# Optimization experiments

Hardware: AMD Instinct MI355X
Metric: run time of the kernel (lower is better)

Reference implementation:

```python
import jax, jax.numpy as jnp
import numpy as np

B, P, R_BAR, WIDTH, ADD_WIDTH, KERNEL_WIDTH = 4096, 1024, 64, 1024, 64, 16
NEG_SLOPE = 0.1

def leaky(x):
    return jnp.where(x > 0, x, NEG_SLOPE * x)

def setup_inputs() -> dict:
    key = jax.random.key(0)
    ks = jax.random.split(key, 16)
    s = lambda fan_in: 1.0 / np.sqrt(fan_in)
    return {
        "x": jax.random.normal(ks[0], (B, P), jnp.float32),
        # PCA layer 1: Linear(p -> r_bar), stored [in, out]
        "W_pca": jax.random.normal(ks[1], (P, R_BAR), jnp.float32) * s(P),
        "b_pca": jnp.zeros((R_BAR,), jnp.float32),
        # relu_stack: Linear(r_bar -> width), Linear(width -> width)
        "W1": jax.random.normal(ks[2], (R_BAR, WIDTH), jnp.float32) * s(R_BAR),
        "b1": jnp.zeros((WIDTH,), jnp.float32),
        "W2": jax.random.normal(ks[3], (WIDTH, WIDTH), jnp.float32) * s(WIDTH),
        "b2": jnp.zeros((WIDTH,), jnp.float32),
        # AdditiveLayer 1: r_bar tiny Linears (kernel_width -> add_width), batched [r, in, out]
        "add1_W": jax.random.normal(ks[4], (R_BAR, KERNEL_WIDTH, ADD_WIDTH), jnp.float32) * s(KERNEL_WIDTH),
        "add1_b": jnp.zeros((R_BAR, ADD_WIDTH), jnp.float32),
        "add1_bias": jnp.zeros((1,), jnp.float32),
        # AdditiveLayer 2: r_bar Linears (add_width -> add_width)
        "add2_W": jax.random.normal(ks[5], (R_BAR, ADD_WIDTH, ADD_WIDTH), jnp.float32) * s(ADD_WIDTH),
        "add2_b": jnp.zeros((R_BAR, ADD_WIDTH), jnp.float32),
        "add2_bias": jnp.zeros((1,), jnp.float32),
        # PCA layer 2: Linear(r_bar*add_width -> r_bar)
        "W_pca2": jax.random.normal(ks[6], (R_BAR * ADD_WIDTH, R_BAR), jnp.float32) * s(R_BAR * ADD_WIDTH),
        "b_pca2": jnp.zeros((R_BAR,), jnp.float32),
        # last layer: Linear(r_bar -> 1)
        "W_last": jax.random.normal(ks[7], (R_BAR, 1), jnp.float32) * s(R_BAR),
        "b_last": jnp.zeros((1,), jnp.float32),
    }

def reference(x, W_pca, b_pca, W1, b1, W2, b2,
              add1_W, add1_b, add1_bias,
              add2_W, add2_b, add2_bias,
              W_pca2, b_pca2, W_last, b_last):
    # PcaLayer 1 (cov/trace bookkeeping does not affect the output)
    t = x @ W_pca + b_pca                                   # [B, r_bar]
    # relu_stack (nn_depth = 2)
    h = leaky(t @ W1 + b1)                                   # [B, width]
    h = leaky(h @ W2 + b2)                                   # [B, width]
    # AdditiveLayer 1: modulo-gather kernel_width cols per slot, batched tiny GEMMs
    idx1 = jnp.arange(R_BAR * KERNEL_WIDTH) % h.shape[1]
    g1 = h[:, idx1].reshape(-1, R_BAR, KERNEL_WIDTH)         # [B, r, kw]
    a = jnp.einsum('brk,rko->bro', g1, add1_W) + add1_b      # [B, r, add_w]
    a = leaky(a.reshape(a.shape[0], -1) + add1_bias)         # [B, r*add_w]
    # AdditiveLayer 2: slices are contiguous (mod is identity) -> plain reshape
    g2 = a.reshape(-1, R_BAR, ADD_WIDTH)
    a2 = jnp.einsum('bri,rio->bro', g2, add2_W) + add2_b
    a2 = leaky(a2.reshape(a2.shape[0], -1) + add2_bias)      # [B, r*add_w]
    # PcaLayer 2 + last layer
    t2 = a2 @ W_pca2 + b_pca2                                # [B, r_bar]
    out = (t2 @ W_last + b_last).reshape(-1, 1)              # [B, 1]
    return out
```

## Files before the change

### kernel.cpp

```cpp
#include <hip/hip_runtime.h>

#define NEG_SLOPE 0.1f

__device__ __forceinline__ float leaky(float v) { return v > 0.0f ? v : NEG_SLOPE * v; }

typedef _Float16 h4_t __attribute__((ext_vector_type(4)));
typedef _Float16 h8_t __attribute__((ext_vector_type(8)));
typedef float f32x4 __attribute__((ext_vector_type(4)));

__device__ __forceinline__ unsigned lds_off(const void* p) {
    return (unsigned)(unsigned long long)p;
}

__device__ __forceinline__ void lgkm0() {
    asm volatile("s_waitcnt lgkmcnt(0)" ::: "memory");
    __builtin_amdgcn_sched_barrier(0);
}

__device__ __forceinline__ h4_t tr16(unsigned addr) {
    h4_t d;
    asm volatile("ds_read_b64_tr_b16 %0, %1" : "=v"(d) : "v"(addr) : "memory");
    return d;
}

__global__ __launch_bounds__(256) void prep_and_splitk(const float* __restrict__ W2,
                                                       const float* __restrict__ W1,
                                                       const float* __restrict__ a1W,
                                                       const float* __restrict__ a2W,
                                                       const float* __restrict__ Wp2,
                                                       const float* __restrict__ x,
                                                       const float* __restrict__ Wpca,
                                                       _Float16* __restrict__ W2T,
                                                       _Float16* __restrict__ W1T,
                                                       _Float16* __restrict__ wpack,
                                                       float* __restrict__ P)
{
    __shared__ float tile[32][33];
    __shared__ alignas(16) float As[32][33];
    __shared__ alignas(16) float Bs[32][64];
    const int b   = blockIdx.x;
    const int tid = threadIdx.x;

    if (b < 1024) {
        const int n0 = (b & 31) * 32, k0 = (b >> 5) * 32;
        const int r = tid >> 3, c4 = (tid & 7) * 4;
        float4 v = *reinterpret_cast<const float4*>(&W2[(size_t)(k0 + r) * 1024 + n0 + c4]);
        tile[r][c4 + 0] = v.x; tile[r][c4 + 1] = v.y;
        tile[r][c4 + 2] = v.z; tile[r][c4 + 3] = v.w;
        __syncthreads();
        h4_t o;
        o[0] = (_Float16)tile[c4 + 0][r]; o[1] = (_Float16)tile[c4 + 1][r];
        o[2] = (_Float16)tile[c4 + 2][r]; o[3] = (_Float16)tile[c4 + 3][r];
        *reinterpret_cast<h4_t*>(&W2T[(size_t)(n0 + r) * 1024 + k0 + c4]) = o;
    } else if (b < 1088) {
        const int b2 = b - 1024;
        const int n0 = (b2 & 31) * 32, k0 = (b2 >> 5) * 32;
        const int r = tid >> 3, c4 = (tid & 7) * 4;
        float4 v = *reinterpret_cast<const float4*>(&W1[(size_t)(k0 + r) * 1024 + n0 + c4]);
        tile[r][c4 + 0] = v.x; tile[r][c4 + 1] = v.y;
        tile[r][c4 + 2] = v.z; tile[r][c4 + 3] = v.w;
        __syncthreads();
        h4_t o;
        o[0] = (_Float16)tile[c4 + 0][r]; o[1] = (_Float16)tile[c4 + 1][r];
        o[2] = (_Float16)tile[c4 + 2][r]; o[3] = (_Float16)tile[c4 + 3][r];
        *reinterpret_cast<h4_t*>(&W1T[(size_t)(n0 + r) * 64 + k0 + c4]) = o;
    } else if (b < 3392) {
        const int idx = (b - 1088) * 256 + tid;
        if (idx < 589824) {
            const int r = idx / 9216, qq = idx % 9216;
            float v;
            if (qq < 1024) {
                int nt = qq >> 8, rem = qq & 255, l = rem >> 2, j = rem & 3;
                int n = nt * 16 + (l & 15), k = (l >> 4) * 4 + j;
                v = a1W[(size_t)r * 1024 + k * 64 + n];
            } else if (qq < 5120) {
                int p = qq - 1024, kt = p >> 11, u = p & 2047, nt = u >> 9, s = u & 511,
                    l = s >> 3, j = s & 7;
                int n = nt * 16 + (l & 15), k = kt * 32 + (l >> 4) * 8 + j;
                v = a2W[(size_t)r * 4096 + k * 64 + n];
            } else {
                int p = qq - 5120, kt = p >> 11, u = p & 2047, nt = u >> 9, s = u & 511,
                    l = s >> 3, j = s & 7;
                int n = nt * 16 + (l & 15), k = kt * 32 + (l >> 4) * 8 + j;
                v = Wp2[((size_t)r * 64 + k) * 64 + n];
            }
            wpack[idx] = (_Float16)v;
        }
    } else {
        const int b2    = b - 3392;
        const int row0  = (b2 & 127) * 32;
        const int kbase = (b2 >> 7) * 128;
        const int r0    = (tid >> 4) * 2;
        const int c0    = (tid & 15) * 4;
        const int am    = tid >> 3;
        const int ak    = (tid & 7) * 4;
        float acc[2][4] = {};

#pragma unroll
        for (int kc = 0; kc < 128; kc += 32) {
            const int k0 = kbase + kc;
            float4 va = *reinterpret_cast<const float4*>(&x[(size_t)(row0 + am) * 1024 + k0 + ak]);
            As[ak + 0][am] = va.x; As[ak + 1][am] = va.y;
            As[ak + 2][am] = va.z; As[ak + 3][am] = va.w;
#pragma unroll
            for (int p = 0; p < 2; ++p) {
                int idx = tid + p * 256;
                int kk  = idx >> 4;
                int nq  = (idx & 15) * 4;
                *reinterpret_cast<float4*>(&Bs[kk][nq]) =
                    *reinterpret_cast<const float4*>(&Wpca[(size_t)(k0 + kk) * 64 + nq]);
            }
            __syncthreads();
#pragma unroll
            for (int k = 0; k < 32; ++k) {
                float a0 = As[k][r0], a1 = As[k][r0 + 1];
                float4 bv = *reinterpret_cast<const float4*>(&Bs[k][c0]);
                acc[0][0] = fmaf(a0, bv.x, acc[0][0]); acc[0][1] = fmaf(a0, bv.y, acc[0][1]);
                acc[0][2] = fmaf(a0, bv.z, acc[0][2]); acc[0][3] = fmaf(a0, bv.w, acc[0][3]);
                acc[1][0] = fmaf(a1, bv.x, acc[1][0]); acc[1][1] = fmaf(a1, bv.y, acc[1][1]);
                acc[1][2] = fmaf(a1, bv.z, acc[1][2]); acc[1][3] = fmaf(a1, bv.w, acc[1][3]);
            }
            __syncthreads();
        }
#pragma unroll
        for (int i = 0; i < 2; ++i) {
            float4 o; o.x = acc[i][0]; o.y = acc[i][1]; o.z = acc[i][2]; o.w = acc[i][3];
            *reinterpret_cast<float4*>(
                &P[((size_t)(b2 >> 7) * 4096 + row0 + r0 + i) * 64 + c0]) = o;
        }
    }
}

__global__ __launch_bounds__(256) void combine_t16(const float* __restrict__ P,
                                                   const float* __restrict__ bias,
                                                   _Float16* __restrict__ t16)
{
    const int idx = blockIdx.x * 256 + threadIdx.x;
    float s = bias[idx & 63];
#pragma unroll
    for (int c = 0; c < 8; ++c)
        s += P[(size_t)c * 262144 + idx];
    t16[idx] = (_Float16)s;
}

__global__ __launch_bounds__(256) void gemm_k64_mfma(const _Float16* __restrict__ A,
                                                     const _Float16* __restrict__ BT,
                                                     const float* __restrict__ bias,
                                                     _Float16* __restrict__ C)
{
    __shared__ alignas(16) _Float16 As[128 * 64];
    __shared__ alignas(16) _Float16 Bs[128 * 64];
    const int tid = threadIdx.x;
    const int l   = tid & 63;
    const int w   = tid >> 6;
    const int wm  = w >> 1;
    const int wn  = w & 1;
    const int bm0 = blockIdx.y * 128;
    const int bn0 = blockIdx.x * 128;
    const int fr  = l & 15;
    const int fg  = l >> 4;
    const int srow  = l >> 3;
    const int sslot = l & 7;

#pragma unroll
    for (int i = 0; i < 4; ++i) {
        const int r0   = w * 32 + i * 8;
        const int rowA = r0 + srow;
        const int slot = sslot ^ (rowA & 7);
        __builtin_amdgcn_global_load_lds(
            (const __attribute__((address_space(1))) void*)&A[(size_t)(bm0 + rowA) * 64 + slot * 8],
            (__attribute__((address_space(3))) void*)&As[r0 * 64], 16, 0, 0);
        __builtin_amdgcn_global_load_lds(
            (const __attribute__((address_space(1))) void*)&BT[(size_t)(bn0 + rowA) * 64 + slot * 8],
            (__attribute__((address_space(3))) void*)&Bs[r0 * 64], 16, 0, 0);
    }
    __syncthreads();

    f32x4 acc[4][4] = {};
#pragma unroll
    for (int ks = 0; ks < 2; ++ks) {
        h8_t af[4], bf[4];
#pragma unroll
        for (int mt = 0; mt < 4; ++mt) {
            int row = wm * 64 + mt * 16 + fr;
            int sg  = ks * 4 + fg;
            af[mt] = *reinterpret_cast<const h8_t*>(&As[row * 64 + ((sg ^ (row & 7)) << 3)]);
        }
#pragma unroll
        for (int nt = 0; nt < 4; ++nt) {
            int row = wn * 64 + nt * 16 + fr;
            int sg  = ks * 4 + fg;
            bf[nt] = *reinterpret_cast<const h8_t*>(&Bs[row * 64 + ((sg ^ (row & 7)) << 3)]);
        }
#pragma unroll
        for (int mt = 0; mt < 4; ++mt)
#pragma unroll
            for (int nt = 0; nt < 4; ++nt)
                acc[mt][nt] = __builtin_amdgcn_mfma_f32_16x16x32_f16(af[mt], bf[nt],
                                                                     acc[mt][nt], 0, 0, 0);
    }

#pragma unroll
    for (int nt = 0; nt < 4; ++nt) {
        const int col = bn0 + wn * 64 + nt * 16 + fr;
        const float bv = bias[col];
#pragma unroll
        for (int mt = 0; mt < 4; ++mt)
#pragma unroll
            for (int rg = 0; rg < 4; ++rg) {
                const int row = bm0 + wm * 64 + mt * 16 + fg * 4 + rg;
                float v = acc[mt][nt][rg] + bv;
                C[(size_t)row * 1024 + col] = (_Float16)fmaxf(v, NEG_SLOPE * v);
            }
    }
}

__global__ __launch_bounds__(256) void gemm_mfma_f16_v2(const _Float16* __restrict__ A,
                                                        const _Float16* __restrict__ BT,
                                                        const float* __restrict__ bias,
                                                        _Float16* __restrict__ h2t)
{
    __shared__ alignas(16) _Float16 As[64 * 64];
    __shared__ alignas(16) _Float16 Bs[128 * 64];
    const int tid = threadIdx.x;
    const int l   = tid & 63;
    const int w   = tid >> 6;
    const int wm  = w >> 1;
    const int wn  = w & 1;
    const int bm0 = blockIdx.y * 64;
    const int bn0 = blockIdx.x * 128;
    const int fr  = l & 15;
    const int fg  = l >> 4;
    const int srow  = l >> 3;
    const int sslot = l & 7;

    f32x4 acc[2][4] = {};

    for (int k0 = 0; k0 < 1024; k0 += 64) {
#pragma unroll
        for (int i = 0; i < 2; ++i) {
            const int r0   = w * 16 + i * 8;
            const int rowA = r0 + srow;
            const int slot = sslot ^ (rowA & 7);
            __builtin_amdgcn_global_load_lds(
                (const __attribute__((address_space(1))) void*)&A[(size_t)(bm0 + rowA) * 1024 + k0 + slot * 8],
                (__attribute__((address_space(3))) void*)&As[r0 * 64], 16, 0, 0);
        }
#pragma unroll
        for (int i = 0; i < 4; ++i) {
            const int r0   = w * 32 + i * 8;
            const int rowB = r0 + srow;
            const int slot = sslot ^ (rowB & 7);
            __builtin_amdgcn_global_load_lds(
                (const __attribute__((address_space(1))) void*)&BT[(size_t)(bn0 + rowB) * 1024 + k0 + slot * 8],
                (__attribute__((address_space(3))) void*)&Bs[r0 * 64], 16, 0, 0);
        }
        __syncthreads();

#pragma unroll
        for (int ks = 0; ks < 2; ++ks) {
            h8_t af[2], bf[4];
#pragma unroll
            for (int mt = 0; mt < 2; ++mt) {
                int row = wm * 32 + mt * 16 + fr;
                int sg  = ks * 4 + fg;
                af[mt] = *reinterpret_cast<const h8_t*>(&As[row * 64 + ((sg ^ (row & 7)) << 3)]);
            }
#pragma unroll
            for (int nt = 0; nt < 4; ++nt) {
                int row = wn * 64 + nt * 16 + fr;
                int sg  = ks * 4 + fg;
                bf[nt] = *reinterpret_cast<const h8_t*>(&Bs[row * 64 + ((sg ^ (row & 7)) << 3)]);
            }
#pragma unroll
            for (int mt = 0; mt < 2; ++mt)
#pragma unroll
                for (int nt = 0; nt < 4; ++nt)
                    acc[mt][nt] = __builtin_amdgcn_mfma_f32_16x16x32_f16(af[mt], bf[nt],
                                                                         acc[mt][nt], 0, 0, 0);
        }
        __syncthreads();
    }

    const int rblk0 = (bm0 >> 4) + wm * 2;
    const int cblk0 = (bn0 >> 4) + wn * 4;
#pragma unroll
    for (int nt = 0; nt < 4; ++nt) {
        const int col = bn0 + wn * 64 + nt * 16 + fr;
        const float bv = bias[col];
#pragma unroll
        for (int mt = 0; mt < 2; ++mt) {
            h4_t pk;
#pragma unroll
            for (int r = 0; r < 4; ++r) {
                float v = acc[mt][nt][r] + bv;
                pk[r] = (_Float16)fmaxf(v, NEG_SLOPE * v);
            }
            *reinterpret_cast<h4_t*>(
                &h2t[(((size_t)(cblk0 + nt) * 256 + rblk0 + mt) * 16 + fr) * 16 + fg * 4]) = pk;
        }
    }
}

#define RCH 4

__global__ __launch_bounds__(256) void fused_tail5(const _Float16* __restrict__ h2t,
                                                   const _Float16* __restrict__ wpack,
                                                   const float* __restrict__ a1b,
                                                   const float* __restrict__ a1bias,
                                                   const float* __restrict__ a2b,
                                                   const float* __restrict__ a2bias,
                                                   float* __restrict__ partials)
{
    __shared__ alignas(16) _Float16 stage[2][11264];
    __shared__ alignas(16) _Float16 act[4][2048];

    const int tid = threadIdx.x;
    const int l = tid & 63, w = tid >> 6;
    const int c = l & 15, q = l >> 4;
    const int row0  = blockIdx.x * 128;
    const int rbase = blockIdx.y * RCH;
    const float b1s = a1bias[0], b2s = a2bias[0];

    const unsigned trl   = l * 8;
    const unsigned abase = lds_off(&act[w][0]);

    float b1v[RCH][4], b2v[RCH][4];
#pragma unroll
    for (int rl = 0; rl < RCH; ++rl)
#pragma unroll
        for (int nt = 0; nt < 4; ++nt) {
            b1v[rl][nt] = a1b[(rbase + rl) * 64 + nt * 16 + c] + b1s;
            b2v[rl][nt] = a2b[(rbase + rl) * 64 + nt * 16 + c] + b2s;
        }

    auto STAGE = [&](int rl, int b) {
        const int r = rbase + rl;
        const _Float16* hsrc = h2t + ((size_t)r * 256 + blockIdx.x * 8) * 256;
        const _Float16* wsrc = wpack + (size_t)r * 9216;
#pragma unroll
        for (int i = 0; i < 6; ++i) {
            const int ch = i * 4 + w;
            if (ch < 22) {
                const _Float16* src = (ch < 4) ? (hsrc + ch * 512) : (wsrc + (ch - 4) * 512);
                __builtin_amdgcn_global_load_lds(
                    (const __attribute__((address_space(1))) void*)(src + l * 8),
                    (__attribute__((address_space(3))) void*)&stage[b][ch * 512], 16, 0, 0);
            }
        }
    };

    STAGE(0, 0);
    __syncthreads();

    f32x4 accT[2][4] = {};
    int cur = 0;

#pragma unroll
    for (int rl = 0; rl < RCH; ++rl) {
        if (rl + 1 < RCH) STAGE(rl + 1, cur ^ 1);

        const _Float16* sp = &stage[cur][0];
        const unsigned sbytes = lds_off(sp);

        h4_t ha0 = tr16(sbytes + (unsigned)(w) * 512 + trl);
        h4_t ha1 = tr16(sbytes + (unsigned)(w + 4) * 512 + trl);
        lgkm0();
        f32x4 pa[2][4];
#pragma unroll
        for (int nt = 0; nt < 4; ++nt) {
            h4_t bf = *reinterpret_cast<const h4_t*>(&sp[2048 + nt * 256 + l * 4]);
            pa[0][nt] = __builtin_amdgcn_mfma_f32_16x16x16f16(ha0, bf, (f32x4){0.f,0.f,0.f,0.f}, 0, 0, 0);
            pa[1][nt] = __builtin_amdgcn_mfma_f32_16x16x16f16(ha1, bf, (f32x4){0.f,0.f,0.f,0.f}, 0, 0, 0);
        }
#pragma unroll
        for (int j = 0; j < 2; ++j)
#pragma unroll
            for (int nt = 0; nt < 4; ++nt) {
                h4_t pk;
#pragma unroll
                for (int rg = 0; rg < 4; ++rg) {
                    float v = pa[j][nt][rg] + b1v[rl][nt];
                    pk[rg] = (_Float16)fmaxf(v, NEG_SLOPE * v);
                }
                const int kk = nt * 16 + c;
                const int hh = (kk >> 2) & 1;
                const int kp = (kk & 3) | ((kk >> 3) << 2);
                *reinterpret_cast<h4_t*>(&act[w][j * 1024 + hh * 512 + kp * 16 + q * 4]) = pk;
            }
        lgkm0();

        h8_t afB[2][2];
#pragma unroll
        for (int j = 0; j < 2; ++j)
#pragma unroll
            for (int kt = 0; kt < 2; ++kt) {
                h4_t lo = tr16(abase + (unsigned)(j * 2048 + kt * 512) + trl);
                h4_t hi = tr16(abase + (unsigned)(j * 2048 + 1024 + kt * 512) + trl);
                afB[j][kt] = __builtin_shufflevector(lo, hi, 0, 1, 2, 3, 4, 5, 6, 7);
            }
        lgkm0();
        f32x4 pb[2][4] = {};
#pragma unroll
        for (int kt = 0; kt < 2; ++kt)
#pragma unroll
            for (int nt = 0; nt < 4; ++nt) {
                h8_t bf = *reinterpret_cast<const h8_t*>(&sp[3072 + kt * 2048 + nt * 512 + l * 8]);
                pb[0][nt] = __builtin_amdgcn_mfma_f32_16x16x32_f16(afB[0][kt], bf, pb[0][nt], 0, 0, 0);
                pb[1][nt] = __builtin_amdgcn_mfma_f32_16x16x32_f16(afB[1][kt], bf, pb[1][nt], 0, 0, 0);
            }
#pragma unroll
        for (int j = 0; j < 2; ++j)
#pragma unroll
            for (int nt = 0; nt < 4; ++nt) {
                h4_t pk;
#pragma unroll
                for (int rg = 0; rg < 4; ++rg) {
                    float v = pb[j][nt][rg] + b2v[rl][nt];
                    pk[rg] = (_Float16)fmaxf(v, NEG_SLOPE * v);
                }
                const int kk = nt * 16 + c;
                const int hh = (kk >> 2) & 1;
                const int kp = (kk & 3) | ((kk >> 3) << 2);
                *reinterpret_cast<h4_t*>(&act[w][j * 1024 + hh * 512 + kp * 16 + q * 4]) = pk;
            }
        lgkm0();

        h8_t afC[2][2];
#pragma unroll
        for (int j = 0; j < 2; ++j)
#pragma unroll
            for (int kt = 0; kt < 2; ++kt) {
                h4_t lo = tr16(abase + (unsigned)(j * 2048 + kt * 512) + trl);
                h4_t hi = tr16(abase + (unsigned)(j * 2048 + 1024 + kt * 512) + trl);
                afC[j][kt] = __builtin_shufflevector(lo, hi, 0, 1, 2, 3, 4, 5, 6, 7);
            }
        lgkm0();
#pragma unroll
        for (int kt = 0; kt < 2; ++kt)
#pragma unroll
            for (int nt = 0; nt < 4; ++nt) {
                h8_t bf = *reinterpret_cast<const h8_t*>(&sp[7168 + kt * 2048 + nt * 512 + l * 8]);
                accT[0][nt] = __builtin_amdgcn_mfma_f32_16x16x32_f16(afC[0][kt], bf, accT[0][nt], 0, 0, 0);
                accT[1][nt] = __builtin_amdgcn_mfma_f32_16x16x32_f16(afC[1][kt], bf, accT[1][nt], 0, 0, 0);
            }

        __syncthreads();
        cur ^= 1;
    }

#pragma unroll
    for (int j = 0; j < 2; ++j)
#pragma unroll
        for (int nt = 0; nt < 4; ++nt)
#pragma unroll
            for (int rg = 0; rg < 4; ++rg)
                partials[((size_t)blockIdx.y * 4096 + row0 + (w + 4 * j) * 16 + q * 4 + rg) * 64
                         + nt * 16 + c] = accT[j][nt][rg];
}

__global__ __launch_bounds__(256) void reduce_out(const float* __restrict__ partials,
                                                  const float* __restrict__ bp2,
                                                  const float* __restrict__ Wl,
                                                  const float* __restrict__ bl,
                                                  float* __restrict__ out)
{
    const int tid = threadIdx.x;
    const int row = blockIdx.x * 4 + (tid >> 6);
    const int col = tid & 63;
    float s = bp2[col];
#pragma unroll
    for (int c = 0; c < 16; ++c)
        s += partials[(size_t)c * 262144 + (size_t)row * 64 + col];
    s *= Wl[col];
    s += __shfl_xor(s, 1);
    s += __shfl_xor(s, 2);
    s += __shfl_xor(s, 4);
    s += __shfl_xor(s, 8);
    s += __shfl_xor(s, 16);
    s += __shfl_xor(s, 32);
    if (col == 0) out[row] = s + bl[0];
}

extern "C" void kernel_launch(void* const* d_in, const int* in_sizes, int n_in,
                              void* d_out, int out_size, void* d_ws, size_t ws_size,
                              hipStream_t stream)
{
    const float* x      = (const float*)d_in[0];
    const float* Wpca   = (const float*)d_in[1];
    const float* bpca   = (const float*)d_in[2];
    const float* W1     = (const float*)d_in[3];
    const float* b1     = (const float*)d_in[4];
    const float* W2     = (const float*)d_in[5];
    const float* b2     = (const float*)d_in[6];
    const float* a1W    = (const float*)d_in[7];
    const float* a1b    = (const float*)d_in[8];
    const float* a1bias = (const float*)d_in[9];
    const float* a2W    = (const float*)d_in[10];
    const float* a2b    = (const float*)d_in[11];
    const float* a2bias = (const float*)d_in[12];
    const float* Wp2    = (const float*)d_in[13];
    const float* bp2    = (const float*)d_in[14];
    const float* Wl     = (const float*)d_in[15];
    const float* bl     = (const float*)d_in[16];
    float* out = (float*)d_out;

    char* wsb = (char*)d_ws;
    _Float16* t16      = (_Float16*)(wsb);
    _Float16* h1h      = (_Float16*)(wsb + (1ull  << 20));
    _Float16* h2t      = (_Float16*)(wsb + (9ull  << 20));
    _Float16* W2T      = (_Float16*)(wsb + (17ull << 20));
    _Float16* wpack    = (_Float16*)(wsb + (19ull << 20));
    _Float16* W1T      = (_Float16*)(wsb + (21ull << 20));
    float*    partials = (float*)   (wsb + (22ull << 20));
    float*    tpart    = (float*)   (wsb + (9ull  << 20));

    prep_and_splitk<<<dim3(4416), 256, 0, stream>>>(W2, W1, a1W, a2W, Wp2, x, Wpca,
                                                    W2T, W1T, wpack, tpart);
    combine_t16<<<dim3(1024), 256, 0, stream>>>(tpart, bpca, t16);
    gemm_k64_mfma<<<dim3(8, 32), 256, 0, stream>>>(t16, W1T, b1, h1h);
    gemm_mfma_f16_v2<<<dim3(8, 64), 256, 0, stream>>>(h1h, W2T, b2, h2t);
    fused_tail5<<<dim3(32, 16), 256, 0, stream>>>(h2t, wpack, a1b, a1bias,
                                                  a2b, a2bias, partials);
    reduce_out<<<dim3(1024), 256, 0, stream>>>(partials, bp2, Wl, bl, out);
}
```

Measured before the change: 67.14 us.

## Fuse final reduction and last layer into tail kernel via atomics

The tail kernel now projects its split-r partial PCA2 outputs through W_last inside the kernel. It reduces them across lanes with shuffles and atomically adds a scalar per row into the output. The output is pre-initialised with the constant bias term (b_last + bp2·Wl) inside the earlier combine kernel. This removes the 16 MB partials write/read and the reduce_out launch, at the cost of 16-way float atomic contention per row and nondeterministic summation order.

Result: faster. 63.95 us (-4.8%).

```diff
diff --git a/kernel.cpp b/kernel.cpp
--- a/kernel.cpp
+++ b/kernel.cpp
@@ -133,7 +133,11 @@
 
 __global__ __launch_bounds__(256) void combine_t16(const float* __restrict__ P,
                                                    const float* __restrict__ bias,
-                                                   _Float16* __restrict__ t16)
+                                                   const float* __restrict__ bp2,
+                                                   const float* __restrict__ Wl,
+                                                   const float* __restrict__ bl,
+                                                   _Float16* __restrict__ t16,
+                                                   float* __restrict__ out)
 {
     const int idx = blockIdx.x * 256 + threadIdx.x;
     float s = bias[idx & 63];
@@ -141,6 +145,14 @@
     for (int c = 0; c < 8; ++c)
         s += P[(size_t)c * 262144 + idx];
     t16[idx] = (_Float16)s;
+
+    if (idx < 4096) {
+        float cst = bl[0];
+#pragma unroll
+        for (int f = 0; f < 64; ++f)
+            cst += bp2[f] * Wl[f];
+        out[idx] = cst;
+    }
 }
 
 __global__ __launch_bounds__(256) void gemm_k64_mfma(const _Float16* __restrict__ A,
@@ -304,13 +316,14 @@
 
 #define RCH 4
 
-__global__ __launch_bounds__(256) void fused_tail5(const _Float16* __restrict__ h2t,
-                                                   const _Float16* __restrict__ wpack,
-                                                   const float* __restrict__ a1b,
-                                                   const float* __restrict__ a1bias,
-                                                   const float* __restrict__ a2b,
-                                                   const float* __restrict__ a2bias,
-                                                   float* __restrict__ partials)
+__global__ __launch_bounds__(256) void fused_tail5b(const _Float16* __restrict__ h2t,
+                                                    const _Float16* __restrict__ wpack,
+                                                    const float* __restrict__ a1b,
+                                                    const float* __restrict__ a1bias,
+                                                    const float* __restrict__ a2b,
+                                                    const float* __restrict__ a2bias,
+                                                    const float* __restrict__ Wl,
+                                                    float* __restrict__ out)
 {
     __shared__ alignas(16) _Float16 stage[2][11264];
     __shared__ alignas(16) _Float16 act[4][2048];
@@ -333,6 +346,9 @@
             b1v[rl][nt] = a1b[(rbase + rl) * 64 + nt * 16 + c] + b1s;
             b2v[rl][nt] = a2b[(rbase + rl) * 64 + nt * 16 + c] + b2s;
         }
+    float wlv[4];
+#pragma unroll
+    for (int nt = 0; nt < 4; ++nt) wlv[nt] = Wl[nt * 16 + c];
 
     auto STAGE = [&](int rl, int b) {
         const int r = rbase + rl;
@@ -452,34 +468,18 @@
 #pragma unroll
     for (int j = 0; j < 2; ++j)
 #pragma unroll
-        for (int nt = 0; nt < 4; ++nt)
-#pragma unroll
-            for (int rg = 0; rg < 4; ++rg)
-                partials[((size_t)blockIdx.y * 4096 + row0 + (w + 4 * j) * 16 + q * 4 + rg) * 64
-                         + nt * 16 + c] = accT[j][nt][rg];
-}
-
-__global__ __launch_bounds__(256) void reduce_out(const float* __restrict__ partials,
-                                                  const float* __restrict__ bp2,
-                                                  const float* __restrict__ Wl,
-                                                  const float* __restrict__ bl,
-                                                  float* __restrict__ out)
-{
-    const int tid = threadIdx.x;
-    const int row = blockIdx.x * 4 + (tid >> 6);
-    const int col = tid & 63;
-    float s = bp2[col];
-#pragma unroll
-    for (int c = 0; c < 16; ++c)
-        s += partials[(size_t)c * 262144 + (size_t)row * 64 + col];
-    s *= Wl[col];
-    s += __shfl_xor(s, 1);
-    s += __shfl_xor(s, 2);
-    s += __shfl_xor(s, 4);
-    s += __shfl_xor(s, 8);
-    s += __shfl_xor(s, 16);
-    s += __shfl_xor(s, 32);
-    if (col == 0) out[row] = s + bl[0];
+        for (int rg = 0; rg < 4; ++rg) {
+            float s = accT[j][0][rg] * wlv[0] + accT[j][1][rg] * wlv[1] +
+                      accT[j][2][rg] * wlv[2] + accT[j][3][rg] * wlv[3];
+            s += __shfl_xor(s, 1);
+            s += __shfl_xor(s, 2);
+            s += __shfl_xor(s, 4);
+            s += __shfl_xor(s, 8);
+            if (c == 0) {
+                const int row = row0 + (w + 4 * j) * 16 + q * 4 + rg;
+                atomicAdd(&out[row], s);
+            }
+        }
 }
 
 extern "C" void kernel_launch(void* const* d_in, const int* in_sizes, int n_in,
@@ -506,21 +506,19 @@
     float* out = (float*)d_out;
 
     char* wsb = (char*)d_ws;
-    _Float16* t16      = (_Float16*)(wsb);
-    _Float16* h1h      = (_Float16*)(wsb + (1ull  << 20));
-    _Float16* h2t      = (_Float16*)(wsb + (9ull  << 20));
-    _Float16* W2T      = (_Float16*)(wsb + (17ull << 20));
-    _Float16* wpack    = (_Float16*)(wsb + (19ull << 20));
-    _Float16* W1T      = (_Float16*)(wsb + (21ull << 20));
-    float*    partials = (float*)   (wsb + (22ull << 20));
-    float*    tpart    = (float*)   (wsb + (9ull  << 20));
+    _Float16* t16   = (_Float16*)(wsb);
+    _Float16* h1h   = (_Float16*)(wsb + (1ull  << 20));
+    _Float16* h2t   = (_Float16*)(wsb + (9ull  << 20));
+    _Float16* W2T   = (_Float16*)(wsb + (17ull << 20));
+    _Float16* wpack = (_Float16*)(wsb + (19ull << 20));
+    _Float16* W1T   = (_Float16*)(wsb + (21ull << 20));
+    float*    tpart = (float*)   (wsb + (9ull  << 20));
 
     prep_and_splitk<<<dim3(4416), 256, 0, stream>>>(W2, W1, a1W, a2W, Wp2, x, Wpca,
                                                     W2T, W1T, wpack, tpart);
-    combine_t16<<<dim3(1024), 256, 0, stream>>>(tpart, bpca, t16);
+    combine_t16<<<dim3(1024), 256, 0, stream>>>(tpart, bpca, bp2, Wl, bl, t16, out);
     gemm_k64_mfma<<<dim3(8, 32), 256, 0, stream>>>(t16, W1T, b1, h1h);
     gemm_mfma_f16_v2<<<dim3(8, 64), 256, 0, stream>>>(h1h, W2T, b2, h2t);
-    fused_tail5<<<dim3(32, 16), 256, 0, stream>>>(h2t, wpack, a1b, a1bias,
-                                                  a2b, a2bias, partials);
-    reduce_out<<<dim3(1024), 256, 0, stream>>>(partials, bp2, Wl, bl, out);
-}
+    fused_tail5b<<<dim3(32, 16), 256, 0, stream>>>(h2t, wpack, a1b, a1bias,
+                                                   a2b, a2bias, Wl, out);
+}
```
